# Performance work log

Measured on AMD Instinct MI355X. Metric: run time of the kernel, lower is better.

## Reference

```python
import jax, jax.numpy as jnp
import numpy as np

N = 50000        # nodes
E = 800000       # edges (avg degree 16)
NODE_D = 128     # node_attr_dim
EDGE_D = 16      # edge_attr_dim
HID = 300        # hidden_dim (module default)


def setup_inputs() -> dict:
    key = jax.random.key(0)
    ks = jax.random.split(key, 8)
    x = jax.random.normal(ks[0], (N, NODE_D), jnp.float32)
    edge_attr = jax.random.normal(ks[1], (E, EDGE_D), jnp.float32)
    edge_weight = jax.random.uniform(ks[2], (E,), jnp.float32)
    node_weight = jax.random.uniform(ks[3], (N,), jnp.float32)
    edge_index = jax.random.randint(ks[4], (2, E), 0, N, jnp.int32)
    # lin0: Linear(node_attr_dim + edge_attr_dim, hidden_dim)
    W0 = jax.random.normal(ks[5], (NODE_D + EDGE_D, HID), jnp.float32) / np.sqrt(NODE_D + EDGE_D)
    b0 = jnp.zeros((HID,), jnp.float32)
    # mp_layer.linear: Linear(hidden_dim, hidden_dim)
    W = jax.random.normal(ks[6], (HID, HID), jnp.float32) / np.sqrt(HID)
    b = jnp.zeros((HID,), jnp.float32)
    return dict(x=x, edge_attr=edge_attr, edge_weight=edge_weight,
                node_weight=node_weight, W0=W0, b0=b0, W=W, b=b,
                edge_index=edge_index)


def reference(x, edge_attr, edge_weight, node_weight, W0, b0, W, b, edge_index):
    src = edge_index[0]   # x_j (source, flow='source_to_target')
    dst = edge_index[1]   # aggregation target i
    n = x.shape[0]

    # --- isFirstLayer: weighted sum of incoming edge features, scattered at dst ---
    inc = jax.ops.segment_sum(edge_weight[:, None] * edge_attr, dst, num_segments=n)  # [N, EDGE_D]
    h0 = jax.nn.relu(jnp.concatenate([x, inc], axis=1) @ W0 + b0)                     # [N, HID]

    # --- MessagePassingLayer: message = edge_weight * x_j; aggr = mean at dst ---
    msg = edge_weight[:, None] * h0[src]                                              # [E, HID]
    agg = jax.ops.segment_sum(msg, dst, num_segments=n)                               # [N, HID]
    deg = jax.ops.segment_sum(jnp.ones((src.shape[0],), x.dtype), dst, num_segments=n)
    agg = agg / jnp.maximum(deg, 1.0)[:, None]  # scatter-mean (0 where no incoming edges)

    # --- update: relu(h0 + linear(aggr)) (add_residual=True) ---
    h = jax.nn.relu(h0 + agg @ W + b)
    # isLastLayer=False -> no node_weight scaling
    return (h, h0)
```

## Files before the change

kernel.cpp:

```cpp
#include <hip/hip_runtime.h>

#define NN 50000
#define NE 800000
#define ND 128
#define ED 16
#define HID 300
#define KP1 192
#define KP2 320
#define NP 320

#define SCAN_T 256
#define SCAN_B ((NN + SCAN_T - 1) / SCAN_T)

typedef __attribute__((ext_vector_type(8))) short short8;
typedef __attribute__((ext_vector_type(4))) float f32x4;

__device__ __forceinline__ unsigned short f2b(float f) {
    unsigned int u = __float_as_uint(f);
    u = (u + 0x7FFFu + ((u >> 16) & 1u)) >> 16;
    return (unsigned short)u;
}
__device__ __forceinline__ float blo(unsigned int u) {
    return __uint_as_float(u << 16);
}
__device__ __forceinline__ float bhi(unsigned int u) {
    return __uint_as_float(u & 0xffff0000u);
}

__device__ __forceinline__ void gload16(const void* g, void* l) {
    __builtin_amdgcn_global_load_lds(
        (const __attribute__((address_space(1))) void*)g,
        (__attribute__((address_space(3))) void*)l, 16, 0, 0);
}

__device__ __forceinline__ int block_iscan(int v, int tid) {
    int lane = tid & 63;
    #pragma unroll
    for (int off = 1; off < 64; off <<= 1) {
        int t = __shfl_up(v, off);
        if (lane >= off) v += t;
    }
    __shared__ int wsum[4];
    int wid = tid >> 6;
    if (lane == 63) wsum[wid] = v;
    __syncthreads();
    int add = 0;
    #pragma unroll
    for (int w = 0; w < 4; ++w)
        if (w < wid) add += wsum[w];
    return v + add;
}

__global__ void hist_kernel(const int* __restrict__ ei, int* __restrict__ rowptr) {
    int e = blockIdx.x * blockDim.x + threadIdx.x;
    if (e < NE) atomicAdd(&rowptr[ei[NE + e] + 1], 1);
}

__global__ __launch_bounds__(SCAN_T) void scan1(int* __restrict__ rowptr,
                                                int* __restrict__ blockSums) {
    int i = blockIdx.x * SCAN_T + threadIdx.x;
    int v = (i < NN) ? rowptr[1 + i] : 0;
    v = block_iscan(v, threadIdx.x);
    if (i < NN) rowptr[1 + i] = v;
    if (threadIdx.x == SCAN_T - 1) blockSums[blockIdx.x] = v;
}

__global__ __launch_bounds__(SCAN_T) void scan2(int* __restrict__ blockSums) {
    int t = threadIdx.x;
    int orig = (t < SCAN_B) ? blockSums[t] : 0;
    int v = block_iscan(orig, t);
    if (t < SCAN_B) blockSums[t] = v - orig;
}

__global__ __launch_bounds__(SCAN_T) void scan3(int* __restrict__ rowptr,
                                                const int* __restrict__ blockSums,
                                                int* __restrict__ cursor) {
    int i = blockIdx.x * SCAN_T + threadIdx.x;
    if (i < NN) {
        int v = rowptr[1 + i] + blockSums[blockIdx.x];
        rowptr[1 + i] = v;
        if (i + 1 < NN) cursor[i + 1] = v;
    }
    if (i == 0) cursor[0] = 0;
}

__global__ void fill_kernel(const int* __restrict__ ei, const float* __restrict__ ew,
                            int* __restrict__ cursor, uint2* __restrict__ csr_sw,
                            uint2* __restrict__ csr_ew) {
    int e = blockIdx.x * blockDim.x + threadIdx.x;
    if (e < NE) {
        int d = ei[NE + e];
        int pos = atomicAdd(&cursor[d], 1);
        unsigned int wb = __float_as_uint(ew[e]);
        uint2 sw; sw.x = (unsigned int)ei[e]; sw.y = wb;
        uint2 ee; ee.x = (unsigned int)e;     ee.y = wb;
        csr_sw[pos] = sw;
        csr_ew[pos] = ee;
    }
}

__global__ __launch_bounds__(256) void cast_x(const float* __restrict__ x,
                                              unsigned short* __restrict__ A1) {
    int tid = blockIdx.x * blockDim.x + threadIdx.x;
    if (tid >= NN * 32) return;
    int n = tid >> 5, q = tid & 31;
    float4 v = *(const float4*)&x[(size_t)n * ND + q * 4];
    unsigned short o[4] = {f2b(v.x), f2b(v.y), f2b(v.z), f2b(v.w)};
    *(uint2*)&A1[(size_t)n * KP1 + q * 4] = *(uint2*)o;
}

__global__ __launch_bounds__(256) void inc_kernel(
    const float* __restrict__ edge_attr,
    const int* __restrict__ rowptr,
    const uint2* __restrict__ csr_ew,
    unsigned short* __restrict__ A1) {
    int n = (blockIdx.x * blockDim.x + threadIdx.x) >> 6;
    int lane = threadIdx.x & 63;
    if (n >= NN) return;
    int g = lane >> 4, j = lane & 15;
    int lo = rowptr[n], hi = rowptr[n + 1];
    float v = 0.f;
    for (int k = lo + g; k < hi; k += 4) {
        uint2 ewp = csr_ew[k];
        float w = __uint_as_float(ewp.y);
        v += w * edge_attr[(size_t)ewp.x * ED + j];
    }
    v += __shfl_xor(v, 16);
    v += __shfl_xor(v, 32);
    if (lane < 16)
        A1[(size_t)n * KP1 + ND + lane] = f2b(v);
    else
        A1[(size_t)n * KP1 + ND + lane] = 0;
}

__global__ void castB0(const float* __restrict__ W0, unsigned short* __restrict__ B0T) {
    int n = blockIdx.x, k = threadIdx.x;
    float v = (n < HID && k < ND + ED) ? W0[(size_t)k * HID + n] : 0.f;
    B0T[(size_t)n * KP1 + k] = f2b(v);
}

__global__ void castB(const float* __restrict__ W, unsigned short* __restrict__ BT) {
    int n = blockIdx.x, k = threadIdx.x;
    float v = (n < HID && k < HID) ? W[(size_t)k * HID + n] : 0.f;
    BT[(size_t)n * KP2 + k] = f2b(v);
}

template <int MODE, int KP>
__global__ __launch_bounds__(256) void gemm_mfma(
    const unsigned short* __restrict__ A,
    const unsigned short* __restrict__ BT,
    const float* __restrict__ bias,
    const float* __restrict__ RES,
    float* __restrict__ C,
    unsigned short* __restrict__ h0b,
    int M)
{
    __shared__ unsigned short As[128][64];
    __shared__ unsigned short Bs[160][64];
    const int tid = threadIdx.x;
    const int m0 = blockIdx.x * 128;
    const int n0 = blockIdx.y * 160;
    const int wave = tid >> 6, lane = tid & 63;
    const int wm = wave >> 1, wn = wave & 1;
    const int quad = lane >> 4, lr = lane & 15;
    const int lr8 = lane >> 3;
    const int lc8 = (lane & 7) * 8;
    f32x4 acc[4][5] = {};

    for (int kb = 0; kb < KP; kb += 64) {
        #pragma unroll
        for (int i = 0; i < 4; ++i) {
            int r = wave * 32 + i * 8;
            int mg = m0 + r + lr8; if (mg >= M) mg = M - 1;
            gload16(&A[(size_t)mg * KP + kb + lc8], &As[0][0] + r * 64);
        }
        #pragma unroll
        for (int i = 0; i < 5; ++i) {
            int r = wave * 40 + i * 8;
            gload16(&BT[(size_t)(n0 + r + lr8) * KP + kb + lc8], &Bs[0][0] + r * 64);
        }
        __syncthreads();
        #pragma unroll
        for (int ks = 0; ks < 2; ++ks) {
            short8 a[4], b[5];
            #pragma unroll
            for (int tm = 0; tm < 4; ++tm)
                a[tm] = *(const short8*)&As[wm * 64 + tm * 16 + lr][ks * 32 + quad * 8];
            #pragma unroll
            for (int tn = 0; tn < 5; ++tn)
                b[tn] = *(const short8*)&Bs[wn * 80 + tn * 16 + lr][ks * 32 + quad * 8];
            #pragma unroll
            for (int tm = 0; tm < 4; ++tm)
                #pragma unroll
                for (int tn = 0; tn < 5; ++tn)
                    acc[tm][tn] = __builtin_amdgcn_mfma_f32_16x16x32_bf16(
                        a[tm], b[tn], acc[tm][tn], 0, 0, 0);
        }
        __syncthreads();
    }
    #pragma unroll
    for (int tm = 0; tm < 4; ++tm) {
        #pragma unroll
        for (int tn = 0; tn < 5; ++tn) {
            int ng = n0 + wn * 80 + tn * 16 + lr;
            #pragma unroll
            for (int r = 0; r < 4; ++r) {
                int mg = m0 + wm * 64 + tm * 16 + quad * 4 + r;
                if (mg < M && ng < HID) {
                    float v = acc[tm][tn][r] + bias[ng];
                    if (MODE == 1) v += RES[(size_t)mg * HID + ng];
                    v = fmaxf(v, 0.f);
                    C[(size_t)mg * HID + ng] = v;
                    if (MODE == 0) h0b[(size_t)mg * NP + ng] = f2b(v);
                }
            }
        }
    }
}

__global__ __launch_bounds__(256) void agg_kernel(
    const unsigned short* __restrict__ h0b,
    const int* __restrict__ rowptr,
    const uint2* __restrict__ csr_sw,
    unsigned short* __restrict__ aggB)
{
    int n = (blockIdx.x * blockDim.x + threadIdx.x) >> 6;
    int lane = threadIdx.x & 63;
    if (n >= NN) return;
    int lo = rowptr[n], hi = rowptr[n + 1];
    float acc[8] = {};
    const uint4* h4 = (const uint4*)h0b;
    bool act = lane < 40;
    int k = lo;
    for (; k + 1 < hi; k += 2) {
        uint2 p0 = csr_sw[k], p1 = csr_sw[k + 1];
        int s0 = (int)p0.x, s1 = (int)p1.x;
        float w0 = __uint_as_float(p0.y), w1 = __uint_as_float(p1.y);
        uint4 r0 = {0, 0, 0, 0}, r1 = {0, 0, 0, 0};
        if (act) {
            r0 = h4[(size_t)s0 * 40 + lane];
            r1 = h4[(size_t)s1 * 40 + lane];
        }
        acc[0] += w0 * blo(r0.x); acc[1] += w0 * bhi(r0.x);
        acc[2] += w0 * blo(r0.y); acc[3] += w0 * bhi(r0.y);
        acc[4] += w0 * blo(r0.z); acc[5] += w0 * bhi(r0.z);
        acc[6] += w0 * blo(r0.w); acc[7] += w0 * bhi(r0.w);
        acc[0] += w1 * blo(r1.x); acc[1] += w1 * bhi(r1.x);
        acc[2] += w1 * blo(r1.y); acc[3] += w1 * bhi(r1.y);
        acc[4] += w1 * blo(r1.z); acc[5] += w1 * bhi(r1.z);
        acc[6] += w1 * blo(r1.w); acc[7] += w1 * bhi(r1.w);
    }
    if (k < hi) {
        uint2 p0 = csr_sw[k];
        int s0 = (int)p0.x;
        float w0 = __uint_as_float(p0.y);
        uint4 r0 = {0, 0, 0, 0};
        if (act) r0 = h4[(size_t)s0 * 40 + lane];
        acc[0] += w0 * blo(r0.x); acc[1] += w0 * bhi(r0.x);
        acc[2] += w0 * blo(r0.y); acc[3] += w0 * bhi(r0.y);
        acc[4] += w0 * blo(r0.z); acc[5] += w0 * bhi(r0.z);
        acc[6] += w0 * blo(r0.w); acc[7] += w0 * bhi(r0.w);
    }
    if (act) {
        float invd = 1.f / fmaxf((float)(hi - lo), 1.f);
        int cbase = lane * 8;
        unsigned int o[4];
        #pragma unroll
        for (int i = 0; i < 4; ++i) {
            int c0 = cbase + 2 * i, c1 = c0 + 1;
            unsigned int ulo = (c0 < HID) ? f2b(acc[2 * i] * invd) : 0;
            unsigned int uhi = (c1 < HID) ? f2b(acc[2 * i + 1] * invd) : 0;
            o[i] = ulo | (uhi << 16);
        }
        uint4* a4 = (uint4*)aggB;
        uint4 v; v.x = o[0]; v.y = o[1]; v.z = o[2]; v.w = o[3];
        a4[(size_t)n * 40 + lane] = v;
    }
}

extern "C" void kernel_launch(void* const* d_in, const int* in_sizes, int n_in,
                              void* d_out, int out_size, void* d_ws, size_t ws_size,
                              hipStream_t stream) {
    const float* x           = (const float*)d_in[0];
    const float* edge_attr   = (const float*)d_in[1];
    const float* edge_weight = (const float*)d_in[2];
    const float* W0 = (const float*)d_in[4];
    const float* b0 = (const float*)d_in[5];
    const float* W  = (const float*)d_in[6];
    const float* b  = (const float*)d_in[7];
    const int* ei   = (const int*)d_in[8];

    float* out = (float*)d_out;
    float* h  = out;
    float* h0 = out + (size_t)NN * HID;

    char* p = (char*)d_ws;
    auto alloc = [&](size_t bytes) { char* q = p; p += (bytes + 255) & ~(size_t)255; return q; };
    int*   rowptr  = (int*)  alloc((NN + 1) * sizeof(int));
    int*   cursor  = (int*)  alloc(NN * sizeof(int));
    int*   bsums   = (int*)  alloc(SCAN_B * sizeof(int));
    uint2* csr_sw  = (uint2*)alloc((size_t)NE * sizeof(uint2));
    uint2* csr_ew  = (uint2*)alloc((size_t)NE * sizeof(uint2));
    unsigned short* A1   = (unsigned short*)alloc((size_t)NN * KP1 * 2);
    unsigned short* h0b  = (unsigned short*)alloc((size_t)NN * NP * 2);
    unsigned short* aggB = (unsigned short*)alloc((size_t)NN * NP * 2);
    unsigned short* B0T  = (unsigned short*)alloc((size_t)NP * KP1 * 2);
    unsigned short* BT   = (unsigned short*)alloc((size_t)NP * KP2 * 2);

    hipMemsetAsync(rowptr, 0, (NN + 1) * sizeof(int), stream);
    hist_kernel<<<(NE + 255) / 256, 256, 0, stream>>>(ei, rowptr);
    scan1<<<SCAN_B, SCAN_T, 0, stream>>>(rowptr, bsums);
    scan2<<<1, SCAN_T, 0, stream>>>(bsums);
    scan3<<<SCAN_B, SCAN_T, 0, stream>>>(rowptr, bsums, cursor);
    fill_kernel<<<(NE + 255) / 256, 256, 0, stream>>>(ei, edge_weight, cursor,
                                                      csr_sw, csr_ew);
    castB0<<<NP, KP1, 0, stream>>>(W0, B0T);
    castB<<<NP, KP2, 0, stream>>>(W, BT);
    cast_x<<<(NN * 32 + 255) / 256, 256, 0, stream>>>(x, A1);
    inc_kernel<<<(NN + 3) / 4, 256, 0, stream>>>(edge_attr, rowptr, csr_ew, A1);

    dim3 g((NN + 127) / 128, NP / 160);
    gemm_mfma<0, KP1><<<g, 256, 0, stream>>>(A1, B0T, b0, nullptr, h0, h0b, NN);
    agg_kernel<<<(NN + 3) / 4, 256, 0, stream>>>(h0b, rowptr, csr_sw, aggB);
    gemm_mfma<1, KP2><<<g, 256, 0, stream>>>(aggB, BT, b, h0, h, nullptr, NN);
}
```

Baseline: 529.3 us.

## Double-buffer GEMM LDS tiles and XOR-swizzle to avoid bank conflicts

The MFMA GEMM now keeps two LDS buffers, so the global-to-LDS load of the next K tile is issued before the MFMA work on the current tile. This halves the barriers per K step and overlaps memory with compute. It also XOR-swizzles the 16-byte column chunks on both store and load to cut LDS bank conflicts on the short8 reads. The cost is double the LDS per block, which may lower occupancy. The gains are limited because the GEMMs are a modest share of total time next to the gather and scatter stages.

```diff
diff --git a/kernel.cpp b/kernel.cpp
--- a/kernel.cpp
+++ b/kernel.cpp
@@ -155,8 +155,8 @@
     unsigned short* __restrict__ h0b,
     int M)
 {
-    __shared__ unsigned short As[128][64];
-    __shared__ unsigned short Bs[160][64];
+    __shared__ unsigned short As[2][128][64];
+    __shared__ unsigned short Bs[2][160][64];
     const int tid = threadIdx.x;
     const int m0 = blockIdx.x * 128;
     const int n0 = blockIdx.y * 160;
@@ -164,31 +164,35 @@
     const int wm = wave >> 1, wn = wave & 1;
     const int quad = lane >> 4, lr = lane & 15;
     const int lr8 = lane >> 3;
-    const int lc8 = (lane & 7) * 8;
+    const int lc8 = ((lane & 7) ^ lr8) * 8;
     f32x4 acc[4][5] = {};
 
-    for (int kb = 0; kb < KP; kb += 64) {
+    auto stage = [&](int buf, int kb) {
         #pragma unroll
         for (int i = 0; i < 4; ++i) {
             int r = wave * 32 + i * 8;
             int mg = m0 + r + lr8; if (mg >= M) mg = M - 1;
-            gload16(&A[(size_t)mg * KP + kb + lc8], &As[0][0] + r * 64);
+            gload16(&A[(size_t)mg * KP + kb + lc8], &As[buf][0][0] + r * 64);
         }
         #pragma unroll
         for (int i = 0; i < 5; ++i) {
             int r = wave * 40 + i * 8;
-            gload16(&BT[(size_t)(n0 + r + lr8) * KP + kb + lc8], &Bs[0][0] + r * 64);
-        }
-        __syncthreads();
+            gload16(&BT[(size_t)(n0 + r + lr8) * KP + kb + lc8],
+                    &Bs[buf][0][0] + r * 64);
+        }
+    };
+
+    auto compute = [&](int buf) {
         #pragma unroll
         for (int ks = 0; ks < 2; ++ks) {
+            const int ch = ((ks * 4 + quad) ^ (lr & 7)) * 8;
             short8 a[4], b[5];
             #pragma unroll
             for (int tm = 0; tm < 4; ++tm)
-                a[tm] = *(const short8*)&As[wm * 64 + tm * 16 + lr][ks * 32 + quad * 8];
+                a[tm] = *(const short8*)&As[buf][wm * 64 + tm * 16 + lr][ch];
             #pragma unroll
             for (int tn = 0; tn < 5; ++tn)
-                b[tn] = *(const short8*)&Bs[wn * 80 + tn * 16 + lr][ks * 32 + quad * 8];
+                b[tn] = *(const short8*)&Bs[buf][wn * 80 + tn * 16 + lr][ch];
             #pragma unroll
             for (int tm = 0; tm < 4; ++tm)
                 #pragma unroll
@@ -196,8 +200,21 @@
                     acc[tm][tn] = __builtin_amdgcn_mfma_f32_16x16x32_bf16(
                         a[tm], b[tn], acc[tm][tn], 0, 0, 0);
         }
+    };
+
+    const int NT = KP / 64;
+    stage(0, 0);
+    __syncthreads();
+    int cur = 0;
+    #pragma unroll 1
+    for (int t = 0; t < NT - 1; ++t) {
+        stage(cur ^ 1, (t + 1) * 64);
+        compute(cur);
         __syncthreads();
-    }
+        cur ^= 1;
+    }
+    compute(cur);
+
     #pragma unroll
     for (int tm = 0; tm < 4; ++tm) {
         #pragma unroll
```

New measurement: 523.9 us. No clear change (-1.0%).

## Load GEMM MFMA operands directly from global memory, bypassing LDS staging

Applied to the files above, without the earlier changes.

The bf16 GEMM kernel drops its shared-memory tiles and global_load_lds staging. Each lane now reads its short8 A and B fragments straight from global memory (L1/L2) inside a fully unrolled K loop, with no __syncthreads. Occupancy is raised to 3 blocks per SIMD via launch_bounds. This removes the LDS round-trip and the barriers, but the reads become strided 16-byte fragments across rows, which may be poorly coalesced and cause redundant L2 traffic across waves. Register pressure also rises under the tighter launch bounds.

```diff
diff --git a/kernel.cpp b/kernel.cpp
--- a/kernel.cpp
+++ b/kernel.cpp
@@ -25,12 +25,6 @@
 }
 __device__ __forceinline__ float bhi(unsigned int u) {
     return __uint_as_float(u & 0xffff0000u);
-}
-
-__device__ __forceinline__ void gload16(const void* g, void* l) {
-    __builtin_amdgcn_global_load_lds(
-        (const __attribute__((address_space(1))) void*)g,
-        (__attribute__((address_space(3))) void*)l, 16, 0, 0);
 }
 
 __device__ __forceinline__ int block_iscan(int v, int tid) {
@@ -146,7 +140,7 @@
 }
 
 template <int MODE, int KP>
-__global__ __launch_bounds__(256) void gemm_mfma(
+__global__ __launch_bounds__(256, 3) void gemm_mfma(
     const unsigned short* __restrict__ A,
     const unsigned short* __restrict__ BT,
     const float* __restrict__ bias,
@@ -155,49 +149,45 @@
     unsigned short* __restrict__ h0b,
     int M)
 {
-    __shared__ unsigned short As[128][64];
-    __shared__ unsigned short Bs[160][64];
     const int tid = threadIdx.x;
     const int m0 = blockIdx.x * 128;
     const int n0 = blockIdx.y * 160;
     const int wave = tid >> 6, lane = tid & 63;
     const int wm = wave >> 1, wn = wave & 1;
     const int quad = lane >> 4, lr = lane & 15;
-    const int lr8 = lane >> 3;
-    const int lc8 = (lane & 7) * 8;
     f32x4 acc[4][5] = {};
 
-    for (int kb = 0; kb < KP; kb += 64) {
-        #pragma unroll
-        for (int i = 0; i < 4; ++i) {
-            int r = wave * 32 + i * 8;
-            int mg = m0 + r + lr8; if (mg >= M) mg = M - 1;
-            gload16(&A[(size_t)mg * KP + kb + lc8], &As[0][0] + r * 64);
-        }
-        #pragma unroll
-        for (int i = 0; i < 5; ++i) {
-            int r = wave * 40 + i * 8;
-            gload16(&BT[(size_t)(n0 + r + lr8) * KP + kb + lc8], &Bs[0][0] + r * 64);
-        }
-        __syncthreads();
-        #pragma unroll
-        for (int ks = 0; ks < 2; ++ks) {
-            short8 a[4], b[5];
-            #pragma unroll
-            for (int tm = 0; tm < 4; ++tm)
-                a[tm] = *(const short8*)&As[wm * 64 + tm * 16 + lr][ks * 32 + quad * 8];
+    const unsigned short* arow[4];
+    const unsigned short* brow[5];
+    #pragma unroll
+    for (int tm = 0; tm < 4; ++tm) {
+        int mg = m0 + wm * 64 + tm * 16 + lr;
+        if (mg >= M) mg = M - 1;
+        arow[tm] = A + (size_t)mg * KP;
+    }
+    #pragma unroll
+    for (int tn = 0; tn < 5; ++tn)
+        brow[tn] = BT + (size_t)(n0 + wn * 80 + tn * 16 + lr) * KP;
+    const int kc = quad * 8;
+
+    #pragma unroll
+    for (int t = 0; t < KP / 32; ++t) {
+        const int k = t * 32 + kc;
+        short8 a[4], b[5];
+        #pragma unroll
+        for (int tm = 0; tm < 4; ++tm)
+            a[tm] = *(const short8*)&arow[tm][k];
+        #pragma unroll
+        for (int tn = 0; tn < 5; ++tn)
+            b[tn] = *(const short8*)&brow[tn][k];
+        #pragma unroll
+        for (int tm = 0; tm < 4; ++tm)
             #pragma unroll
             for (int tn = 0; tn < 5; ++tn)
-                b[tn] = *(const short8*)&Bs[wn * 80 + tn * 16 + lr][ks * 32 + quad * 8];
-            #pragma unroll
-            for (int tm = 0; tm < 4; ++tm)
-                #pragma unroll
-                for (int tn = 0; tn < 5; ++tn)
-                    acc[tm][tn] = __builtin_amdgcn_mfma_f32_16x16x32_bf16(
-                        a[tm], b[tn], acc[tm][tn], 0, 0, 0);
-        }
-        __syncthreads();
-    }
+                acc[tm][tn] = __builtin_amdgcn_mfma_f32_16x16x32_bf16(
+                    a[tm], b[tn], acc[tm][tn], 0, 0, 0);
+    }
+
     #pragma unroll
     for (int tm = 0; tm < 4; ++tm) {
         #pragma unroll
```

Result: slower. 582.5 us (+10.1%).

## Replace tiled GEMMs with persistent B-resident streaming GEMM using swizzled LDS

Applied to the files above, without the earlier changes.

Both GEMMs now run as persistent blocks that load the whole transposed weight slice (full K) into shared memory once, then stream 32-row A tiles with double buffering while looping over an assigned row range. LDS addresses use an XOR swizzle to avoid bank conflicts, bias is hoisted into registers, and residuals are prefetched before the MFMA loop. This removes the repeated weight reloads and per-K-step barriers of the old 128x160 tiling. In exchange the grids are small fixed sizes (256 and 128x2 blocks), occupancy is limited by the large LDS footprint, and each tile does little MFMA work per barrier.

```diff
diff --git a/kernel.cpp b/kernel.cpp
--- a/kernel.cpp
+++ b/kernel.cpp
@@ -145,8 +145,8 @@
     BT[(size_t)n * KP2 + k] = f2b(v);
 }
 
-template <int MODE, int KP>
-__global__ __launch_bounds__(256) void gemm_mfma(
+template <int MODE, int KP, int BN, int WM, int WN, int RPB>
+__global__ __launch_bounds__(256) void gemm_stream(
     const unsigned short* __restrict__ A,
     const unsigned short* __restrict__ BT,
     const float* __restrict__ bias,
@@ -155,66 +155,117 @@
     unsigned short* __restrict__ h0b,
     int M)
 {
-    __shared__ unsigned short As[128][64];
-    __shared__ unsigned short Bs[160][64];
+    constexpr int CPR = KP / 8;
+    constexpr int ACH = 32 * CPR;
+    constexpr int BCH = BN * CPR;
+    constexpr int AM  = 32 / (16 * WM);
+    constexpr int BNW = BN / (16 * WN);
+    __shared__ unsigned short Bs[BCH * 8];
+    __shared__ unsigned short As[2][ACH * 8];
+
     const int tid = threadIdx.x;
-    const int m0 = blockIdx.x * 128;
-    const int n0 = blockIdx.y * 160;
     const int wave = tid >> 6, lane = tid & 63;
-    const int wm = wave >> 1, wn = wave & 1;
+    const int wm = wave / WN, wn = wave % WN;
     const int quad = lane >> 4, lr = lane & 15;
-    const int lr8 = lane >> 3;
-    const int lc8 = (lane & 7) * 8;
-    f32x4 acc[4][5] = {};
-
-    for (int kb = 0; kb < KP; kb += 64) {
-        #pragma unroll
-        for (int i = 0; i < 4; ++i) {
-            int r = wave * 32 + i * 8;
-            int mg = m0 + r + lr8; if (mg >= M) mg = M - 1;
-            gload16(&A[(size_t)mg * KP + kb + lc8], &As[0][0] + r * 64);
-        }
-        #pragma unroll
-        for (int i = 0; i < 5; ++i) {
-            int r = wave * 40 + i * 8;
-            gload16(&BT[(size_t)(n0 + r + lr8) * KP + kb + lc8], &Bs[0][0] + r * 64);
-        }
-        __syncthreads();
-        #pragma unroll
-        for (int ks = 0; ks < 2; ++ks) {
-            short8 a[4], b[5];
-            #pragma unroll
-            for (int tm = 0; tm < 4; ++tm)
-                a[tm] = *(const short8*)&As[wm * 64 + tm * 16 + lr][ks * 32 + quad * 8];
-            #pragma unroll
-            for (int tn = 0; tn < 5; ++tn)
-                b[tn] = *(const short8*)&Bs[wn * 80 + tn * 16 + lr][ks * 32 + quad * 8];
-            #pragma unroll
-            for (int tm = 0; tm < 4; ++tm)
+    const int n00 = blockIdx.y * BN;
+    const int rbase = blockIdx.x * RPB;
+    const int rowend = min(rbase + RPB, M);
+    const int nt = (rowend - rbase + 31) >> 5;
+
+    #pragma unroll
+    for (int rd = 0; rd < BCH / 256; ++rd) {
+        int s = rd * 256 + tid;
+        int row = s / CPR, c = s - row * CPR;
+        int cs = (c & ~7) | ((c & 7) ^ (row & 7));
+        gload16(&BT[(size_t)(n00 + row) * KP + cs * 8], &Bs[s * 8]);
+    }
+    auto stageA = [&](int buf, int mb) {
+        #pragma unroll
+        for (int rd = 0; rd < ACH / 256; ++rd) {
+            int s = rd * 256 + tid;
+            int row = s / CPR, c = s - row * CPR;
+            int cs = (c & ~7) | ((c & 7) ^ (row & 7));
+            int mg = mb + row; if (mg >= M) mg = M - 1;
+            gload16(&A[(size_t)mg * KP + cs * 8], &As[buf][s * 8]);
+        }
+    };
+    stageA(0, rbase);
+
+    float bias_r[BNW];
+    #pragma unroll
+    for (int tn = 0; tn < BNW; ++tn) {
+        int ng = n00 + wn * (BNW * 16) + tn * 16 + lr;
+        bias_r[tn] = (ng < HID) ? bias[ng] : 0.f;
+    }
+    __syncthreads();
+
+    int cur = 0;
+    #pragma unroll 1
+    for (int t = 0; t < nt; ++t) {
+        const int mb = rbase + t * 32;
+        if (t + 1 < nt) stageA(cur ^ 1, mb + 32);
+
+        float res_r[AM][BNW][4];
+        if (MODE == 1) {
+            #pragma unroll
+            for (int tm = 0; tm < AM; ++tm)
+            #pragma unroll
+            for (int tn = 0; tn < BNW; ++tn) {
+                int ng = n00 + wn * (BNW * 16) + tn * 16 + lr;
+                int ngc = ng < HID ? ng : HID - 1;
                 #pragma unroll
-                for (int tn = 0; tn < 5; ++tn)
+                for (int r = 0; r < 4; ++r) {
+                    int mg = mb + (wm * AM + tm) * 16 + quad * 4 + r;
+                    int mgc = mg < M ? mg : M - 1;
+                    res_r[tm][tn][r] = RES[(size_t)mgc * HID + ngc];
+                }
+            }
+        }
+
+        f32x4 acc[AM][BNW] = {};
+        const int rm = lr & 7;
+        #pragma unroll
+        for (int tt = 0; tt < KP / 32; ++tt) {
+            int cA = tt * 4 + quad;
+            int sw8 = ((cA & ~7) | ((cA & 7) ^ rm)) * 8;
+            short8 a[AM], b[BNW];
+            #pragma unroll
+            for (int tm = 0; tm < AM; ++tm) {
+                int ar = (wm * AM + tm) * 16 + lr;
+                a[tm] = *(const short8*)&As[cur][ar * KP + sw8];
+            }
+            #pragma unroll
+            for (int tn = 0; tn < BNW; ++tn) {
+                int br = wn * (BNW * 16) + tn * 16 + lr;
+                b[tn] = *(const short8*)&Bs[br * KP + sw8];
+            }
+            #pragma unroll
+            for (int tm = 0; tm < AM; ++tm)
+                #pragma unroll
+                for (int tn = 0; tn < BNW; ++tn)
                     acc[tm][tn] = __builtin_amdgcn_mfma_f32_16x16x32_bf16(
                         a[tm], b[tn], acc[tm][tn], 0, 0, 0);
         }
-        __syncthreads();
-    }
-    #pragma unroll
-    for (int tm = 0; tm < 4; ++tm) {
-        #pragma unroll
-        for (int tn = 0; tn < 5; ++tn) {
-            int ng = n0 + wn * 80 + tn * 16 + lr;
+
+        #pragma unroll
+        for (int tm = 0; tm < AM; ++tm)
+        #pragma unroll
+        for (int tn = 0; tn < BNW; ++tn) {
+            int ng = n00 + wn * (BNW * 16) + tn * 16 + lr;
             #pragma unroll
             for (int r = 0; r < 4; ++r) {
-                int mg = m0 + wm * 64 + tm * 16 + quad * 4 + r;
-                if (mg < M && ng < HID) {
-                    float v = acc[tm][tn][r] + bias[ng];
-                    if (MODE == 1) v += RES[(size_t)mg * HID + ng];
+                int mg = mb + (wm * AM + tm) * 16 + quad * 4 + r;
+                if (mg < rowend && ng < HID) {
+                    float v = acc[tm][tn][r] + bias_r[tn];
+                    if (MODE == 1) v += res_r[tm][tn][r];
                     v = fmaxf(v, 0.f);
                     C[(size_t)mg * HID + ng] = v;
                     if (MODE == 0) h0b[(size_t)mg * NP + ng] = f2b(v);
                 }
             }
         }
+        __syncthreads();
+        cur ^= 1;
     }
 }
 
@@ -319,8 +370,9 @@
     cast_x<<<(NN * 32 + 255) / 256, 256, 0, stream>>>(x, A1);
     inc_kernel<<<(NN + 3) / 4, 256, 0, stream>>>(edge_attr, rowptr, csr_ew, A1);
 
-    dim3 g((NN + 127) / 128, NP / 160);
-    gemm_mfma<0, KP1><<<g, 256, 0, stream>>>(A1, B0T, b0, nullptr, h0, h0b, NN);
+    gemm_stream<0, KP1, 320, 1, 4, 196><<<dim3(256, 1), 256, 0, stream>>>(
+        A1, B0T, b0, nullptr, h0, h0b, NN);
     agg_kernel<<<(NN + 3) / 4, 256, 0, stream>>>(h0b, rowptr, csr_sw, aggB);
-    gemm_mfma<1, KP2><<<g, 256, 0, stream>>>(aggB, BT, b, h0, h, nullptr, NN);
-}
+    gemm_stream<1, KP2, 160, 2, 2, 391><<<dim3(128, 2), 256, 0, stream>>>(
+        aggB, BT, b, h0, h, nullptr, NN);
+}
```

After: 473.1 us. -10.6%, faster.
